# Kernel optimization log

Measured on AMD Instinct MI355X. Metric: run time of the kernel, lower is better.

Reference implementation:

```python
import jax, jax.numpy as jnp
import numpy as np

N = 50000
E = 400000
NFEAT = 256
NHID = 64
HEADS = [4, 4, 4]
NCLASS = 121
NEG_SLOPE = 0.2


def gat_conv(h, W, al, ar, src, dst, H, D):
    # h: [N, F_in], W: [F_in, H*D], al/ar: [H, D]
    feat = (h @ W).reshape(N, H, D)                    # [N, H, D]
    el = jnp.sum(feat * al[None], axis=-1)             # [N, H]
    er = jnp.sum(feat * ar[None], axis=-1)             # [N, H]
    e = jax.nn.leaky_relu(el[src] + er[dst], NEG_SLOPE)  # [E, H]
    # edge softmax over incoming edges of each dst node
    m = jax.ops.segment_max(e, dst, num_segments=N)    # [N, H]
    ex = jnp.exp(e - m[dst])                           # [E, H]
    s = jax.ops.segment_sum(ex, dst, num_segments=N)   # [N, H]
    alpha = ex / s[dst]                                # [E, H]
    msg = alpha[..., None] * feat[src]                 # [E, H, D]
    return jax.ops.segment_sum(msg, dst, num_segments=N)  # [N, H, D]


def setup_inputs() -> dict:
    key = jax.random.key(0)
    ks = jax.random.split(key, 12)
    d = {
        "h": jax.random.normal(ks[0], (N, NFEAT), dtype=jnp.float32),
        "src": jax.random.randint(ks[1], (E,), 0, N),
        "dst": jax.random.randint(ks[2], (E,), 0, N),
        "W1": jax.random.normal(ks[3], (NFEAT, HEADS[0] * NHID), dtype=jnp.float32) * 0.05,
        "al1": jax.random.normal(ks[4], (HEADS[0], NHID), dtype=jnp.float32) * 0.1,
        "ar1": jax.random.normal(ks[5], (HEADS[0], NHID), dtype=jnp.float32) * 0.1,
        "W2": jax.random.normal(ks[6], (HEADS[0] * NHID, HEADS[1] * NHID), dtype=jnp.float32) * 0.05,
        "al2": jax.random.normal(ks[7], (HEADS[1], NHID), dtype=jnp.float32) * 0.1,
        "ar2": jax.random.normal(ks[8], (HEADS[1], NHID), dtype=jnp.float32) * 0.1,
        "W3": jax.random.normal(ks[9], (HEADS[1] * NHID, HEADS[2] * NCLASS), dtype=jnp.float32) * 0.05,
        "al3": jax.random.normal(ks[10], (HEADS[2], NCLASS), dtype=jnp.float32) * 0.1,
        "ar3": jax.random.normal(ks[11], (HEADS[2], NCLASS), dtype=jnp.float32) * 0.1,
    }
    return d


def reference(h, src, dst, W1, al1, ar1, W2, al2, ar2, W3, al3, ar3):
    # layer 1: [N, H0, NHID] -> flatten -> ELU (norm='none', drop=0, residual='none')
    x = gat_conv(h, W1, al1, ar1, src, dst, HEADS[0], NHID).reshape(N, -1)
    x = jax.nn.elu(x)
    # layer 2
    x = gat_conv(x, W2, al2, ar2, src, dst, HEADS[1], NHID).reshape(N, -1)
    x = jax.nn.elu(x)
    # output layer: mean over heads
    x = gat_conv(x, W3, al3, ar3, src, dst, HEADS[2], NCLASS).mean(axis=1)
    return x
```

## Files before the change

kernel.cpp:

```cpp
#include <hip/hip_runtime.h>
#include <cstddef>

#define NN 50000
#define NE 400000
#define NH 4
#define NC 121
#define MAXSLOT 600000

typedef __attribute__((ext_vector_type(8))) short short8;
typedef __attribute__((ext_vector_type(4))) float f32x4;
typedef __attribute__((ext_vector_type(2))) float f32x2;

static __device__ __forceinline__ unsigned short f2bf(float f) {
    unsigned u = __float_as_uint(f);
    u += 0x7fffu + ((u >> 16) & 1u);
    return (unsigned short)(u >> 16);
}
static __device__ __forceinline__ float bf2f(unsigned short u) {
    return __uint_as_float(((unsigned)u) << 16);
}
static __device__ __forceinline__ f32x2 bfpair(unsigned u) {
    f32x2 r;
    r.x = __uint_as_float(u << 16);
    r.y = __uint_as_float(u & 0xffff0000u);
    return r;
}
static __device__ __forceinline__ void load_lds16(const unsigned short* g, unsigned short* l) {
    __builtin_amdgcn_global_load_lds(
        (const __attribute__((address_space(1))) unsigned*)g,
        (__attribute__((address_space(3))) unsigned*)l, 16, 0, 0);
}

#define PREP_X    3200000
#define PREP_BT1  (PREP_X + 65536)
#define PREP_BT2  (PREP_BT1 + 65536)
#define PREP_CAT  (PREP_BT2 + 131072)
#define PREP_WV   (PREP_CAT + 2048)
#define PREP_END  (PREP_WV + NE)
__global__ __launch_bounds__(256) void prep_k(const float* __restrict__ h,
                                              const float* __restrict__ W1,
                                              const float* __restrict__ W2,
                                              const float* __restrict__ W3,
                                              const float* __restrict__ al3,
                                              const float* __restrict__ ar3,
                                              const int* __restrict__ dst,
                                              unsigned short* __restrict__ h_bf,
                                              unsigned short* __restrict__ BT1,
                                              unsigned short* __restrict__ BT2,
                                              unsigned short* __restrict__ BT3,
                                              float* __restrict__ wl3,
                                              float* __restrict__ wr3,
                                              int* __restrict__ deg) {
    int i = blockIdx.x * blockDim.x + threadIdx.x;
    if (i < PREP_X) {
        float4 v = *(const float4*)&h[(size_t)i * 4];
        ushort4 o;
        o.x = f2bf(v.x); o.y = f2bf(v.y); o.z = f2bf(v.z); o.w = f2bf(v.w);
        *(ushort4*)&h_bf[(size_t)i * 4] = o;
    } else if (i < PREP_BT1) {
        int j = i - PREP_X;
        int n = j >> 8, k = j & 255;
        BT1[j] = f2bf(W1[(size_t)k * 256 + n]);
    } else if (i < PREP_BT2) {
        int j = i - PREP_BT1;
        int n = j >> 8, k = j & 255;
        BT2[j] = f2bf(W2[(size_t)k * 256 + n]);
    } else if (i < PREP_CAT) {
        int j = i - PREP_BT2;
        int np = j >> 8, k = j & 255;
        int hh = np >> 7, c = np & 127;
        float v = (c < NC) ? 0.25f * W3[(size_t)k * 484 + hh * NC + c] : 0.f;
        BT3[j] = f2bf(v);
    } else if (i < PREP_WV) {
        int j = (i - PREP_CAT) & 1023;
        int sel = (i - PREP_CAT) >> 10;
        int hh = j >> 8, k = j & 255;
        const float* a = sel ? ar3 : al3;
        const float* wrow = W3 + (size_t)k * 484 + hh * NC;
        const float* arow = a + hh * NC;
        float s = 0.f;
        for (int d = 0; d < NC; ++d) s += wrow[d] * arow[d];
        if (sel) wr3[j] = s; else wl3[j] = s;
    } else if (i < PREP_END) {
        atomicAdd(&deg[dst[i - PREP_WV]], 1);
    }
}

__global__ __launch_bounds__(256) void gemm_bf16(const unsigned short* __restrict__ A,
                                                 const unsigned short* __restrict__ BT,
                                                 float* __restrict__ Cf,
                                                 unsigned short* __restrict__ Cb,
                                                 const float* __restrict__ al,
                                                 const float* __restrict__ ar,
                                                 float* __restrict__ el,
                                                 float* __restrict__ er,
                                                 int M, int Nout, int K) {
    __shared__ __align__(16) unsigned short Alds[128 * 32];
    __shared__ __align__(16) unsigned short Blds[128 * 32];
    const int tid = threadIdx.x;
    const int wave = tid >> 6;
    const int lane = tid & 63;
    const int quad = lane >> 4;
    const int ml = lane & 15;
    const int m0 = blockIdx.x * 128;
    const int n0 = blockIdx.y * 128;
    const int wm0 = (wave >> 1) * 64;
    const int wn0 = (wave & 1) * 64;

    const unsigned short* Ab = A + (size_t)(m0 + wave * 16 + (lane >> 2)) * K + (lane & 3) * 8;
    const unsigned short* Bb = BT + (size_t)(n0 + wave * 16 + (lane >> 2)) * K + (lane & 3) * 8;
    unsigned short* AldsW = Alds + wave * 512;
    unsigned short* BldsW = Blds + wave * 512;

    f32x4 acc[4][4] = {};

    for (int k0 = 0; k0 < K; k0 += 32) {
        #pragma unroll
        for (int p = 0; p < 2; ++p) {
            load_lds16(Ab + (size_t)(p * 64) * K + k0, AldsW + p * 2048);
            load_lds16(Bb + (size_t)(p * 64) * K + k0, BldsW + p * 2048);
        }
        __syncthreads();

        short8 af[4], bf[4];
        #pragma unroll
        for (int i = 0; i < 4; ++i)
            af[i] = *(const short8*)&Alds[(wm0 + i * 16 + ml) * 32 + quad * 8];
        #pragma unroll
        for (int j = 0; j < 4; ++j)
            bf[j] = *(const short8*)&Blds[(wn0 + j * 16 + ml) * 32 + quad * 8];
        #pragma unroll
        for (int i = 0; i < 4; ++i)
            #pragma unroll
            for (int j = 0; j < 4; ++j)
                acc[i][j] = __builtin_amdgcn_mfma_f32_16x16x32_bf16(af[i], bf[j], acc[i][j], 0, 0, 0);
        __syncthreads();
    }

    #pragma unroll
    for (int i = 0; i < 4; ++i) {
        #pragma unroll
        for (int reg = 0; reg < 4; ++reg) {
            int m = m0 + wm0 + i * 16 + quad * 4 + reg;
            if (m >= M) continue;
            #pragma unroll
            for (int j = 0; j < 4; ++j) {
                int n = n0 + wn0 + j * 16 + ml;
                if (n < Nout) {
                    if (Cb) Cb[(size_t)m * Nout + n] = f2bf(acc[i][j][reg]);
                    else    Cf[(size_t)m * Nout + n] = acc[i][j][reg];
                }
            }
        }
    }

    if (el) {
        int head = (n0 + wn0) >> 6;
        float alv[4], arv[4];
        #pragma unroll
        for (int j = 0; j < 4; ++j) {
            alv[j] = al[head * 64 + j * 16 + ml];
            arv[j] = ar[head * 64 + j * 16 + ml];
        }
        #pragma unroll
        for (int i = 0; i < 4; ++i) {
            #pragma unroll
            for (int reg = 0; reg < 4; ++reg) {
                float sl = 0.f, sr = 0.f;
                #pragma unroll
                for (int j = 0; j < 4; ++j) {
                    float v = acc[i][j][reg];
                    sl += v * alv[j];
                    sr += v * arv[j];
                }
                #pragma unroll
                for (int off = 1; off < 16; off <<= 1) {
                    sl += __shfl_xor(sl, off);
                    sr += __shfl_xor(sr, off);
                }
                int m = m0 + wm0 + i * 16 + quad * 4 + reg;
                if (ml == 0 && m < M) {
                    el[m * 4 + head] = sl;
                    er[m * 4 + head] = sr;
                }
            }
        }
    }
}

__global__ __launch_bounds__(256) void scan1(const int* __restrict__ deg,
                                             int* __restrict__ excl,
                                             int* __restrict__ partials) {
    __shared__ int sh[256];
    int i = blockIdx.x * 256 + threadIdx.x;
    int v = (i < NN) ? ((deg[i] + 3) & ~3) : 0;
    sh[threadIdx.x] = v;
    __syncthreads();
    for (int off = 1; off < 256; off <<= 1) {
        int t = (threadIdx.x >= off) ? sh[threadIdx.x - off] : 0;
        __syncthreads();
        sh[threadIdx.x] += t;
        __syncthreads();
    }
    if (i < NN) excl[i] = sh[threadIdx.x] - v;
    if (threadIdx.x == 255) partials[blockIdx.x] = sh[255];
}

__global__ __launch_bounds__(256) void scan2(int* __restrict__ partials, int nb) {
    __shared__ int sh[256];
    int t = threadIdx.x;
    int v = (t < nb) ? partials[t] : 0;
    sh[t] = v;
    __syncthreads();
    for (int off = 1; off < 256; off <<= 1) {
        int x = (t >= off) ? sh[t - off] : 0;
        __syncthreads();
        sh[t] += x;
        __syncthreads();
    }
    if (t < nb) partials[t] = sh[t] - v;
}

__global__ __launch_bounds__(256) void scan3(const int* __restrict__ excl,
                                             const int* __restrict__ partials,
                                             int* __restrict__ rowptr) {
    int i = blockIdx.x * 256 + threadIdx.x;
    if (i < NN) rowptr[i] = excl[i] + partials[blockIdx.x];
}

__global__ __launch_bounds__(256) void scatter_k(const int* __restrict__ src,
                                                 const int* __restrict__ dst,
                                                 const int* __restrict__ rowptr,
                                                 int* __restrict__ cursor,
                                                 int* __restrict__ ssrc) {
    int e = blockIdx.x * blockDim.x + threadIdx.x;
    if (e >= NE) return;
    int d = dst[e];
    int p = atomicAdd(&cursor[d], 1);
    int pos = rowptr[d] + p;
    ssrc[pos] = src[e] << 9;
}

__global__ __launch_bounds__(256) void agg256(const int* __restrict__ rowptr,
                                              const int* __restrict__ deg,
                                              const int* __restrict__ ssrc,
                                              const float* __restrict__ el,
                                              const float* __restrict__ er,
                                              const unsigned short* __restrict__ feat,
                                              unsigned short* __restrict__ ybf,
                                              const float* __restrict__ wl3,
                                              const float* __restrict__ wr3,
                                              float* __restrict__ el3,
                                              float* __restrict__ er3) {
    int wid = (blockIdx.x * blockDim.x + threadIdx.x) >> 6;
    int lane = threadIdx.x & 63;
    if (wid >= NN) return;
    int n = wid;
    int start = rowptr[n];
    int cnt = deg[n];
    int cnt4 = (cnt + 3) & ~3;
    int head = lane >> 4;
    float ern = er[n * 4 + head];
    const char* elb = (const char*)el + head * 4;
    const char* fbase = (const char*)feat + lane * 8;
    f32x2 a01 = {0.f, 0.f}, a23 = {0.f, 0.f};
    float ssum = 0.f;
    for (int k = 0; k < cnt4; k += 4) {
        int4 sv = *(const int4*)&ssrc[start + k];
        float e0 = *(const float*)(elb + (sv.x >> 5));
        float e1 = *(const float*)(elb + (sv.y >> 5));
        float e2 = *(const float*)(elb + (sv.z >> 5));
        float e3 = *(const float*)(elb + (sv.w >> 5));
        float v0 = e0 + ern; v0 = fmaxf(v0, 0.2f * v0);
        float v1 = e1 + ern; v1 = fmaxf(v1, 0.2f * v1);
        float v2 = e2 + ern; v2 = fmaxf(v2, 0.2f * v2);
        float v3 = e3 + ern; v3 = fmaxf(v3, 0.2f * v3);
        float w0 = (k + 0 < cnt) ? __expf(v0) : 0.f;
        float w1 = (k + 1 < cnt) ? __expf(v1) : 0.f;
        float w2 = (k + 2 < cnt) ? __expf(v2) : 0.f;
        float w3 = (k + 3 < cnt) ? __expf(v3) : 0.f;
        uint2 u0 = *(const uint2*)(fbase + sv.x);
        uint2 u1 = *(const uint2*)(fbase + sv.y);
        uint2 u2 = *(const uint2*)(fbase + sv.z);
        uint2 u3 = *(const uint2*)(fbase + sv.w);
        ssum += (w0 + w1) + (w2 + w3);
        a01 += w0 * bfpair(u0.x); a23 += w0 * bfpair(u0.y);
        a01 += w1 * bfpair(u1.x); a23 += w1 * bfpair(u1.y);
        a01 += w2 * bfpair(u2.x); a23 += w2 * bfpair(u2.y);
        a01 += w3 * bfpair(u3.x); a23 += w3 * bfpair(u3.y);
    }
    float inv = ssum > 0.f ? 1.0f / ssum : 0.f;
    float r0 = a01.x * inv, r1 = a01.y * inv, r2 = a23.x * inv, r3 = a23.y * inv;
    r0 = r0 > 0.f ? r0 : (__expf(r0) - 1.f);
    r1 = r1 > 0.f ? r1 : (__expf(r1) - 1.f);
    r2 = r2 > 0.f ? r2 : (__expf(r2) - 1.f);
    r3 = r3 > 0.f ? r3 : (__expf(r3) - 1.f);
    ushort4 o;
    o.x = f2bf(r0); o.y = f2bf(r1); o.z = f2bf(r2); o.w = f2bf(r3);
    *(ushort4*)&ybf[(size_t)n * 256 + lane * 4] = o;

    if (wl3) {
        float sl[4], sr[4];
        #pragma unroll
        for (int h = 0; h < 4; ++h) {
            float4 a4 = *(const float4*)&wl3[h * 256 + lane * 4];
            float4 b4 = *(const float4*)&wr3[h * 256 + lane * 4];
            sl[h] = r0 * a4.x + r1 * a4.y + r2 * a4.z + r3 * a4.w;
            sr[h] = r0 * b4.x + r1 * b4.y + r2 * b4.z + r3 * b4.w;
        }
        #pragma unroll
        for (int off = 32; off; off >>= 1) {
            #pragma unroll
            for (int h = 0; h < 4; ++h) {
                sl[h] += __shfl_xor(sl[h], off);
                sr[h] += __shfl_xor(sr[h], off);
            }
        }
        if (lane == 0) {
            #pragma unroll
            for (int h = 0; h < 4; ++h) {
                el3[n * 4 + h] = sl[h];
                er3[n * 4 + h] = sr[h];
            }
        }
    }
}

__global__ __launch_bounds__(256) void agg3f(const int* __restrict__ rowptr,
                                             const int* __restrict__ deg,
                                             const int* __restrict__ ssrc,
                                             const float* __restrict__ el,
                                             const float* __restrict__ er,
                                             const unsigned short* __restrict__ feat3,
                                             float* __restrict__ out) {
    int wid = (blockIdx.x * blockDim.x + threadIdx.x) >> 6;
    int lane = threadIdx.x & 63;
    if (wid >= NN) return;
    int n = wid;
    int start = rowptr[n];
    int cnt = deg[n];
    int cnt4 = (cnt + 3) & ~3;
    int head = lane >> 4;
    float ern = er[n * 4 + head];
    const char* elb = (const char*)el + head * 4;
    const char* fbase = (const char*)feat3 + lane * 16;
    f32x2 acc[4] = {};
    float ssum = 0.f;
    for (int k = 0; k < cnt4; k += 4) {
        int4 sv = *(const int4*)&ssrc[start + k];
        float e0 = *(const float*)(elb + (sv.x >> 5));
        float e1 = *(const float*)(elb + (sv.y >> 5));
        float e2 = *(const float*)(elb + (sv.z >> 5));
        float e3 = *(const float*)(elb + (sv.w >> 5));
        uint4 u0 = *(const uint4*)(fbase + ((size_t)(unsigned)sv.x << 1));
        uint4 u1 = *(const uint4*)(fbase + ((size_t)(unsigned)sv.y << 1));
        uint4 u2 = *(const uint4*)(fbase + ((size_t)(unsigned)sv.z << 1));
        uint4 u3 = *(const uint4*)(fbase + ((size_t)(unsigned)sv.w << 1));
        float v0 = e0 + ern; v0 = fmaxf(v0, 0.2f * v0);
        float v1 = e1 + ern; v1 = fmaxf(v1, 0.2f * v1);
        float v2 = e2 + ern; v2 = fmaxf(v2, 0.2f * v2);
        float v3 = e3 + ern; v3 = fmaxf(v3, 0.2f * v3);
        float w0 = (k + 0 < cnt) ? __expf(v0) : 0.f;
        float w1 = (k + 1 < cnt) ? __expf(v1) : 0.f;
        float w2 = (k + 2 < cnt) ? __expf(v2) : 0.f;
        float w3 = (k + 3 < cnt) ? __expf(v3) : 0.f;
        ssum += (w0 + w1) + (w2 + w3);
        acc[0] += w0 * bfpair(u0.x) + w1 * bfpair(u1.x) + w2 * bfpair(u2.x) + w3 * bfpair(u3.x);
        acc[1] += w0 * bfpair(u0.y) + w1 * bfpair(u1.y) + w2 * bfpair(u2.y) + w3 * bfpair(u3.y);
        acc[2] += w0 * bfpair(u0.z) + w1 * bfpair(u1.z) + w2 * bfpair(u2.z) + w3 * bfpair(u3.z);
        acc[3] += w0 * bfpair(u0.w) + w1 * bfpair(u1.w) + w2 * bfpair(u2.w) + w3 * bfpair(u3.w);
    }
    float iv = ssum > 0.f ? 1.f / ssum : 0.f;
    float r[8];
    r[0] = acc[0].x * iv; r[1] = acc[0].y * iv;
    r[2] = acc[1].x * iv; r[3] = acc[1].y * iv;
    r[4] = acc[2].x * iv; r[5] = acc[2].y * iv;
    r[6] = acc[3].x * iv; r[7] = acc[3].y * iv;
    #pragma unroll
    for (int j = 0; j < 8; ++j) {
        r[j] += __shfl_xor(r[j], 16);
        r[j] += __shfl_xor(r[j], 32);
    }
    if (lane < 16) {
        int c0 = lane * 8;
        float* ob = out + (size_t)n * NC + c0;
        #pragma unroll
        for (int j = 0; j < 8; ++j)
            if (c0 + j < NC) ob[j] = r[j];
    }
}

extern "C" void kernel_launch(void* const* d_in, const int* in_sizes, int n_in,
                              void* d_out, int out_size, void* d_ws, size_t ws_size,
                              hipStream_t stream) {
    const float* h   = (const float*)d_in[0];
    const int*   src = (const int*)d_in[1];
    const int*   dst = (const int*)d_in[2];
    const float* W1  = (const float*)d_in[3];
    const float* al1 = (const float*)d_in[4];
    const float* ar1 = (const float*)d_in[5];
    const float* W2  = (const float*)d_in[6];
    const float* al2 = (const float*)d_in[7];
    const float* ar2 = (const float*)d_in[8];
    const float* W3  = (const float*)d_in[9];
    const float* al3 = (const float*)d_in[10];
    const float* ar3 = (const float*)d_in[11];
    float* out = (float*)d_out;

    float* ws = (float*)d_ws;
    unsigned short* x_bf    = (unsigned short*)ws;
    unsigned short* h_bf    = (unsigned short*)(ws + 6400000);
    unsigned short* feat_bf = (unsigned short*)(ws + 12800000);
    unsigned short* feat3   = (unsigned short*)(ws + 6400000);
    float* el  = ws + 32000000;
    float* er  = ws + 32200000;
    float* wl3 = ws + 32400000;
    float* wr3 = ws + 32401024;
    unsigned short* BT1 = (unsigned short*)(ws + 32402048);
    unsigned short* BT2 = (unsigned short*)(ws + 32434816);
    unsigned short* BT3 = (unsigned short*)(ws + 32467584);
    int* ibase  = (int*)(ws + 34933120);
    int* deg      = ibase;
    int* cursor   = ibase + 50000;
    int* excl     = ibase + 100000;
    int* partials = ibase + 150000;
    int* rowptr   = ibase + 150256;
    int* ssrc     = ibase + 200256;
    float* el2 = ws + 36333376;
    float* er2 = ws + 36533376;

    const int NB = (NN + 255) / 256;

    hipMemsetAsync(deg, 0, 2 * NN * sizeof(int), stream);
    hipMemsetAsync(ssrc, 0, MAXSLOT * sizeof(int), stream);

    prep_k<<<(PREP_END + 255) / 256, 256, 0, stream>>>(h, W1, W2, W3, al3, ar3, dst,
                                                       h_bf, BT1, BT2, BT3, wl3, wr3, deg);

    scan1<<<NB, 256, 0, stream>>>(deg, excl, partials);
    scan2<<<1, 256, 0, stream>>>(partials, NB);
    scan3<<<NB, 256, 0, stream>>>(excl, partials, rowptr);
    scatter_k<<<(NE + 255) / 256, 256, 0, stream>>>(src, dst, rowptr, cursor, ssrc);

    dim3 g256((NN + 127) / 128, 2);
    const int WAVE_BLOCKS = (NN * 64 + 255) / 256;

    gemm_bf16<<<g256, 256, 0, stream>>>(h_bf, BT1, nullptr, feat_bf, al1, ar1, el, er, NN, 256, 256);
    agg256<<<WAVE_BLOCKS, 256, 0, stream>>>(rowptr, deg, ssrc, el, er, feat_bf, x_bf,
                                            nullptr, nullptr, nullptr, nullptr);

    gemm_bf16<<<g256, 256, 0, stream>>>(x_bf, BT2, nullptr, feat_bf, al2, ar2, el, er, NN, 256, 256);
    agg256<<<WAVE_BLOCKS, 256, 0, stream>>>(rowptr, deg, ssrc, el, er, feat_bf, x_bf,
                                            wl3, wr3, el2, er2);

    gemm_bf16<<<dim3((NN + 127) / 128, 4), 256, 0, stream>>>(x_bf, BT3, nullptr, feat3,
                                                             nullptr, nullptr, nullptr, nullptr,
                                                             NN, 512, 256);
    agg3f<<<WAVE_BLOCKS, 256, 0, stream>>>(rowptr, deg, ssrc, el2, er2, feat3, out);
}
```

Baseline: 409.3 us.

## Precompute edge attention weights in a separate pass; pad CSR rows to eight

Adds an edge-weight kernel that computes exp(leaky_relu(el[src]+er[dst])) for every padded CSR slot into a head-major array. To do this, scatter now also records each slot's destination, and padding slots are marked with -1 so they get zero weight. The aggregation kernels then read the precomputed weights instead of gathering el and recomputing exp, and their loops process eight neighbours per iteration with rows padded to multiples of eight. This removes the redundant per-lane exp and el gathers and adds memory-level parallelism, at the cost of three extra kernel launches, about 13 MB of extra weight traffic per layer, and a larger padded slot array.

```diff
diff --git a/kernel.cpp b/kernel.cpp
--- a/kernel.cpp
+++ b/kernel.cpp
@@ -5,7 +5,7 @@
 #define NE 400000
 #define NH 4
 #define NC 121
-#define MAXSLOT 600000
+#define SLOT8 800000
 
 typedef __attribute__((ext_vector_type(8))) short short8;
 typedef __attribute__((ext_vector_type(4))) float f32x4;
@@ -15,9 +15,6 @@
     unsigned u = __float_as_uint(f);
     u += 0x7fffu + ((u >> 16) & 1u);
     return (unsigned short)(u >> 16);
-}
-static __device__ __forceinline__ float bf2f(unsigned short u) {
-    return __uint_as_float(((unsigned)u) << 16);
 }
 static __device__ __forceinline__ f32x2 bfpair(unsigned u) {
     f32x2 r;
@@ -193,7 +190,7 @@
                                              int* __restrict__ partials) {
     __shared__ int sh[256];
     int i = blockIdx.x * 256 + threadIdx.x;
-    int v = (i < NN) ? ((deg[i] + 3) & ~3) : 0;
+    int v = (i < NN) ? ((deg[i] + 7) & ~7) : 0;
     sh[threadIdx.x] = v;
     __syncthreads();
     for (int off = 1; off < 256; off <<= 1) {
@@ -232,20 +229,46 @@
                                                  const int* __restrict__ dst,
                                                  const int* __restrict__ rowptr,
                                                  int* __restrict__ cursor,
-                                                 int* __restrict__ ssrc) {
+                                                 int* __restrict__ ssrc,
+                                                 int* __restrict__ sdst) {
     int e = blockIdx.x * blockDim.x + threadIdx.x;
     if (e >= NE) return;
     int d = dst[e];
     int p = atomicAdd(&cursor[d], 1);
     int pos = rowptr[d] + p;
     ssrc[pos] = src[e] << 9;
+    sdst[pos] = d;
+}
+
+__global__ __launch_bounds__(256) void edgew_k(const int* __restrict__ ssrc,
+                                               const int* __restrict__ sdst,
+                                               const float* __restrict__ el,
+                                               const float* __restrict__ er,
+                                               float* __restrict__ wcsr) {
+    int i = blockIdx.x * blockDim.x + threadIdx.x;
+    if (i >= SLOT8) return;
+    int d = sdst[i];
+    float w0 = 0.f, w1 = 0.f, w2 = 0.f, w3 = 0.f;
+    if (d >= 0) {
+        int su = ssrc[i];
+        float4 e_l = *(const float4*)((const char*)el + (su >> 5));
+        float4 e_r = *(const float4*)&er[d * 4];
+        float v0 = e_l.x + e_r.x; v0 = fmaxf(v0, 0.2f * v0);
+        float v1 = e_l.y + e_r.y; v1 = fmaxf(v1, 0.2f * v1);
+        float v2 = e_l.z + e_r.z; v2 = fmaxf(v2, 0.2f * v2);
+        float v3 = e_l.w + e_r.w; v3 = fmaxf(v3, 0.2f * v3);
+        w0 = __expf(v0); w1 = __expf(v1); w2 = __expf(v2); w3 = __expf(v3);
+    }
+    wcsr[0 * SLOT8 + i] = w0;
+    wcsr[1 * SLOT8 + i] = w1;
+    wcsr[2 * SLOT8 + i] = w2;
+    wcsr[3 * SLOT8 + i] = w3;
 }
 
 __global__ __launch_bounds__(256) void agg256(const int* __restrict__ rowptr,
                                               const int* __restrict__ deg,
                                               const int* __restrict__ ssrc,
-                                              const float* __restrict__ el,
-                                              const float* __restrict__ er,
+                                              const float* __restrict__ wcsr,
                                               const unsigned short* __restrict__ feat,
                                               unsigned short* __restrict__ ybf,
                                               const float* __restrict__ wl3,
@@ -257,37 +280,34 @@
     if (wid >= NN) return;
     int n = wid;
     int start = rowptr[n];
-    int cnt = deg[n];
-    int cnt4 = (cnt + 3) & ~3;
+    int cnt8 = (deg[n] + 7) & ~7;
     int head = lane >> 4;
-    float ern = er[n * 4 + head];
-    const char* elb = (const char*)el + head * 4;
+    const float* wp = wcsr + (size_t)head * SLOT8 + start;
     const char* fbase = (const char*)feat + lane * 8;
     f32x2 a01 = {0.f, 0.f}, a23 = {0.f, 0.f};
     float ssum = 0.f;
-    for (int k = 0; k < cnt4; k += 4) {
-        int4 sv = *(const int4*)&ssrc[start + k];
-        float e0 = *(const float*)(elb + (sv.x >> 5));
-        float e1 = *(const float*)(elb + (sv.y >> 5));
-        float e2 = *(const float*)(elb + (sv.z >> 5));
-        float e3 = *(const float*)(elb + (sv.w >> 5));
-        float v0 = e0 + ern; v0 = fmaxf(v0, 0.2f * v0);
-        float v1 = e1 + ern; v1 = fmaxf(v1, 0.2f * v1);
-        float v2 = e2 + ern; v2 = fmaxf(v2, 0.2f * v2);
-        float v3 = e3 + ern; v3 = fmaxf(v3, 0.2f * v3);
-        float w0 = (k + 0 < cnt) ? __expf(v0) : 0.f;
-        float w1 = (k + 1 < cnt) ? __expf(v1) : 0.f;
-        float w2 = (k + 2 < cnt) ? __expf(v2) : 0.f;
-        float w3 = (k + 3 < cnt) ? __expf(v3) : 0.f;
-        uint2 u0 = *(const uint2*)(fbase + sv.x);
-        uint2 u1 = *(const uint2*)(fbase + sv.y);
-        uint2 u2 = *(const uint2*)(fbase + sv.z);
-        uint2 u3 = *(const uint2*)(fbase + sv.w);
-        ssum += (w0 + w1) + (w2 + w3);
-        a01 += w0 * bfpair(u0.x); a23 += w0 * bfpair(u0.y);
-        a01 += w1 * bfpair(u1.x); a23 += w1 * bfpair(u1.y);
-        a01 += w2 * bfpair(u2.x); a23 += w2 * bfpair(u2.y);
-        a01 += w3 * bfpair(u3.x); a23 += w3 * bfpair(u3.y);
+    for (int k = 0; k < cnt8; k += 8) {
+        int4 sa = *(const int4*)&ssrc[start + k];
+        int4 sb = *(const int4*)&ssrc[start + k + 4];
+        float4 wa = *(const float4*)&wp[k];
+        float4 wb = *(const float4*)&wp[k + 4];
+        uint2 u0 = *(const uint2*)(fbase + sa.x);
+        uint2 u1 = *(const uint2*)(fbase + sa.y);
+        uint2 u2 = *(const uint2*)(fbase + sa.z);
+        uint2 u3 = *(const uint2*)(fbase + sa.w);
+        uint2 u4 = *(const uint2*)(fbase + sb.x);
+        uint2 u5 = *(const uint2*)(fbase + sb.y);
+        uint2 u6 = *(const uint2*)(fbase + sb.z);
+        uint2 u7 = *(const uint2*)(fbase + sb.w);
+        ssum += (wa.x + wa.y) + (wa.z + wa.w) + (wb.x + wb.y) + (wb.z + wb.w);
+        a01 += wa.x * bfpair(u0.x); a23 += wa.x * bfpair(u0.y);
+        a01 += wa.y * bfpair(u1.x); a23 += wa.y * bfpair(u1.y);
+        a01 += wa.z * bfpair(u2.x); a23 += wa.z * bfpair(u2.y);
+        a01 += wa.w * bfpair(u3.x); a23 += wa.w * bfpair(u3.y);
+        a01 += wb.x * bfpair(u4.x); a23 += wb.x * bfpair(u4.y);
+        a01 += wb.y * bfpair(u5.x); a23 += wb.y * bfpair(u5.y);
+        a01 += wb.z * bfpair(u6.x); a23 += wb.z * bfpair(u6.y);
+        a01 += wb.w * bfpair(u7.x); a23 += wb.w * bfpair(u7.y);
     }
     float inv = ssum > 0.f ? 1.0f / ssum : 0.f;
     float r0 = a01.x * inv, r1 = a01.y * inv, r2 = a23.x * inv, r3 = a23.y * inv;
@@ -329,8 +349,7 @@
 __global__ __launch_bounds__(256) void agg3f(const int* __restrict__ rowptr,
                                              const int* __restrict__ deg,
                                              const int* __restrict__ ssrc,
-                                             const float* __restrict__ el,
-                                             const float* __restrict__ er,
+                                             const float* __restrict__ wcsr,
                                              const unsigned short* __restrict__ feat3,
                                              float* __restrict__ out) {
     int wid = (blockIdx.x * blockDim.x + threadIdx.x) >> 6;
@@ -338,37 +357,34 @@
     if (wid >= NN) return;
     int n = wid;
     int start = rowptr[n];
-    int cnt = deg[n];
-    int cnt4 = (cnt + 3) & ~3;
+    int cnt8 = (deg[n] + 7) & ~7;
     int head = lane >> 4;
-    float ern = er[n * 4 + head];
-    const char* elb = (const char*)el + head * 4;
+    const float* wp = wcsr + (size_t)head * SLOT8 + start;
     const char* fbase = (const char*)feat3 + lane * 16;
     f32x2 acc[4] = {};
     float ssum = 0.f;
-    for (int k = 0; k < cnt4; k += 4) {
-        int4 sv = *(const int4*)&ssrc[start + k];
-        float e0 = *(const float*)(elb + (sv.x >> 5));
-        float e1 = *(const float*)(elb + (sv.y >> 5));
-        float e2 = *(const float*)(elb + (sv.z >> 5));
-        float e3 = *(const float*)(elb + (sv.w >> 5));
-        uint4 u0 = *(const uint4*)(fbase + ((size_t)(unsigned)sv.x << 1));
-        uint4 u1 = *(const uint4*)(fbase + ((size_t)(unsigned)sv.y << 1));
-        uint4 u2 = *(const uint4*)(fbase + ((size_t)(unsigned)sv.z << 1));
-        uint4 u3 = *(const uint4*)(fbase + ((size_t)(unsigned)sv.w << 1));
-        float v0 = e0 + ern; v0 = fmaxf(v0, 0.2f * v0);
-        float v1 = e1 + ern; v1 = fmaxf(v1, 0.2f * v1);
-        float v2 = e2 + ern; v2 = fmaxf(v2, 0.2f * v2);
-        float v3 = e3 + ern; v3 = fmaxf(v3, 0.2f * v3);
-        float w0 = (k + 0 < cnt) ? __expf(v0) : 0.f;
-        float w1 = (k + 1 < cnt) ? __expf(v1) : 0.f;
-        float w2 = (k + 2 < cnt) ? __expf(v2) : 0.f;
-        float w3 = (k + 3 < cnt) ? __expf(v3) : 0.f;
-        ssum += (w0 + w1) + (w2 + w3);
-        acc[0] += w0 * bfpair(u0.x) + w1 * bfpair(u1.x) + w2 * bfpair(u2.x) + w3 * bfpair(u3.x);
-        acc[1] += w0 * bfpair(u0.y) + w1 * bfpair(u1.y) + w2 * bfpair(u2.y) + w3 * bfpair(u3.y);
-        acc[2] += w0 * bfpair(u0.z) + w1 * bfpair(u1.z) + w2 * bfpair(u2.z) + w3 * bfpair(u3.z);
-        acc[3] += w0 * bfpair(u0.w) + w1 * bfpair(u1.w) + w2 * bfpair(u2.w) + w3 * bfpair(u3.w);
+    for (int k = 0; k < cnt8; k += 8) {
+        int4 sa = *(const int4*)&ssrc[start + k];
+        int4 sb = *(const int4*)&ssrc[start + k + 4];
+        float4 wa = *(const float4*)&wp[k];
+        float4 wb = *(const float4*)&wp[k + 4];
+        uint4 u0 = *(const uint4*)(fbase + ((size_t)(unsigned)sa.x << 1));
+        uint4 u1 = *(const uint4*)(fbase + ((size_t)(unsigned)sa.y << 1));
+        uint4 u2 = *(const uint4*)(fbase + ((size_t)(unsigned)sa.z << 1));
+        uint4 u3 = *(const uint4*)(fbase + ((size_t)(unsigned)sa.w << 1));
+        uint4 u4 = *(const uint4*)(fbase + ((size_t)(unsigned)sb.x << 1));
+        uint4 u5 = *(const uint4*)(fbase + ((size_t)(unsigned)sb.y << 1));
+        uint4 u6 = *(const uint4*)(fbase + ((size_t)(unsigned)sb.z << 1));
+        uint4 u7 = *(const uint4*)(fbase + ((size_t)(unsigned)sb.w << 1));
+        ssum += (wa.x + wa.y) + (wa.z + wa.w) + (wb.x + wb.y) + (wb.z + wb.w);
+        acc[0] += wa.x * bfpair(u0.x) + wa.y * bfpair(u1.x) + wa.z * bfpair(u2.x) + wa.w * bfpair(u3.x);
+        acc[1] += wa.x * bfpair(u0.y) + wa.y * bfpair(u1.y) + wa.z * bfpair(u2.y) + wa.w * bfpair(u3.y);
+        acc[2] += wa.x * bfpair(u0.z) + wa.y * bfpair(u1.z) + wa.z * bfpair(u2.z) + wa.w * bfpair(u3.z);
+        acc[3] += wa.x * bfpair(u0.w) + wa.y * bfpair(u1.w) + wa.z * bfpair(u2.w) + wa.w * bfpair(u3.w);
+        acc[0] += wb.x * bfpair(u4.x) + wb.y * bfpair(u5.x) + wb.z * bfpair(u6.x) + wb.w * bfpair(u7.x);
+        acc[1] += wb.x * bfpair(u4.y) + wb.y * bfpair(u5.y) + wb.z * bfpair(u6.y) + wb.w * bfpair(u7.y);
+        acc[2] += wb.x * bfpair(u4.z) + wb.y * bfpair(u5.z) + wb.z * bfpair(u6.z) + wb.w * bfpair(u7.z);
+        acc[3] += wb.x * bfpair(u4.w) + wb.y * bfpair(u5.w) + wb.z * bfpair(u6.w) + wb.w * bfpair(u7.w);
     }
     float iv = ssum > 0.f ? 1.f / ssum : 0.f;
     float r[8];
@@ -419,20 +435,24 @@
     unsigned short* BT1 = (unsigned short*)(ws + 32402048);
     unsigned short* BT2 = (unsigned short*)(ws + 32434816);
     unsigned short* BT3 = (unsigned short*)(ws + 32467584);
-    int* ibase  = (int*)(ws + 34933120);
+    float* wcsr = ws + 32533120;
+    int* ibase  = (int*)(ws + 35733120);
     int* deg      = ibase;
     int* cursor   = ibase + 50000;
     int* excl     = ibase + 100000;
     int* partials = ibase + 150000;
     int* rowptr   = ibase + 150256;
     int* ssrc     = ibase + 200256;
-    float* el2 = ws + 36333376;
-    float* er2 = ws + 36533376;
+    int* sdst     = ibase + 1000256;
+    float* el2 = ws + 37533376;
+    float* er2 = ws + 37733376;
 
     const int NB = (NN + 255) / 256;
+    const int SLOT_BLOCKS = (SLOT8 + 255) / 256;
 
     hipMemsetAsync(deg, 0, 2 * NN * sizeof(int), stream);
-    hipMemsetAsync(ssrc, 0, MAXSLOT * sizeof(int), stream);
+    hipMemsetAsync(ssrc, 0, SLOT8 * sizeof(int), stream);
+    hipMemsetAsync(sdst, 0xFF, SLOT8 * sizeof(int), stream);
 
     prep_k<<<(PREP_END + 255) / 256, 256, 0, stream>>>(h, W1, W2, W3, al3, ar3, dst,
                                                        h_bf, BT1, BT2, BT3, wl3, wr3, deg);
@@ -440,21 +460,24 @@
     scan1<<<NB, 256, 0, stream>>>(deg, excl, partials);
     scan2<<<1, 256, 0, stream>>>(partials, NB);
     scan3<<<NB, 256, 0, stream>>>(excl, partials, rowptr);
-    scatter_k<<<(NE + 255) / 256, 256, 0, stream>>>(src, dst, rowptr, cursor, ssrc);
+    scatter_k<<<(NE + 255) / 256, 256, 0, stream>>>(src, dst, rowptr, cursor, ssrc, sdst);
 
     dim3 g256((NN + 127) / 128, 2);
     const int WAVE_BLOCKS = (NN * 64 + 255) / 256;
 
     gemm_bf16<<<g256, 256, 0, stream>>>(h_bf, BT1, nullptr, feat_bf, al1, ar1, el, er, NN, 256, 256);
-    agg256<<<WAVE_BLOCKS, 256, 0, stream>>>(rowptr, deg, ssrc, el, er, feat_bf, x_bf,
+    edgew_k<<<SLOT_BLOCKS, 256, 0, stream>>>(ssrc, sdst, el, er, wcsr);
+    agg256<<<WAVE_BLOCKS, 256, 0, stream>>>(rowptr, deg, ssrc, wcsr, feat_bf, x_bf,
                                             nullptr, nullptr, nullptr, nullptr);
 
     gemm_bf16<<<g256, 256, 0, stream>>>(x_bf, BT2, nullptr, feat_bf, al2, ar2, el, er, NN, 256, 256);
-    agg256<<<WAVE_BLOCKS, 256, 0, stream>>>(rowptr, deg, ssrc, el, er, feat_bf, x_bf,
+    edgew_k<<<SLOT_BLOCKS, 256, 0, stream>>>(ssrc, sdst, el, er, wcsr);
+    agg256<<<WAVE_BLOCKS, 256, 0, stream>>>(rowptr, deg, ssrc, wcsr, feat_bf, x_bf,
                                             wl3, wr3, el2, er2);
 
     gemm_bf16<<<dim3((NN + 127) / 128, 4), 256, 0, stream>>>(x_bf, BT3, nullptr, feat3,
                                                              nullptr, nullptr, nullptr, nullptr,
                                                              NN, 512, 256);
-    agg3f<<<WAVE_BLOCKS, 256, 0, stream>>>(rowptr, deg, ssrc, el2, er2, feat3, out);
-}
+    edgew_k<<<SLOT_BLOCKS, 256, 0, stream>>>(ssrc, sdst, el2, er2, wcsr);
+    agg3f<<<WAVE_BLOCKS, 256, 0, stream>>>(rowptr, deg, ssrc, wcsr, feat3, out);
+}
```

Result: slower. 432.2 us (+5.6%).
